# Optimization experiments

Measured on AMD Instinct MI355X. Metric: run time of the kernel, lower is better.

The kernel has to match this reference:

```python
import jax, jax.numpy as jnp
import numpy as np

N = 50000      # nodes
E = 800000     # edges
D_IN = 128
D_H = 128
D_OUT = 64


def _glorot(key, fan_in, fan_out):
    s = float(np.sqrt(6.0 / (fan_in + fan_out)))
    return jax.random.uniform(key, (fan_in, fan_out), jnp.float32, -s, s)


def setup_inputs() -> dict:
    key = jax.random.key(0)
    ks = jax.random.split(key, 8)
    x = jax.random.normal(ks[0], (N, D_IN), jnp.float32)
    edge_index = jax.random.randint(ks[1], (2, E), 0, N, dtype=jnp.int32)
    return {
        "x": x,
        "edge_index": edge_index,
        "W0": _glorot(ks[2], D_IN, D_H), "b0": jnp.zeros((D_H,), jnp.float32),
        "W1": _glorot(ks[3], D_H, D_H),  "b1": jnp.zeros((D_H,), jnp.float32),
        "W2": _glorot(ks[4], D_H, D_H),  "b2": jnp.zeros((D_H,), jnp.float32),
        "W_out": _glorot(ks[5], D_H, D_OUT), "b_out": jnp.zeros((D_OUT,), jnp.float32),
    }


def reference(x, edge_index, W0, b0, W1, b1, W2, b2, W_out, b_out):
    src = edge_index[0]
    dst = edge_index[1]
    # GCN normalization with self-loops: deg = in-degree(dst) + 1
    deg = jax.ops.segment_sum(jnp.ones((E,), x.dtype), dst, num_segments=N) + 1.0
    dinv = jax.lax.rsqrt(deg)                       # [N]
    edge_coef = (dinv[src] * dinv[dst])[:, None]    # [E,1]
    self_coef = (dinv * dinv)[:, None]              # [N,1]

    def gcn_conv(h, W, b):
        h = h @ W                                            # [N,F]
        agg = jax.ops.segment_sum(h[src] * edge_coef, dst, num_segments=N)
        agg = agg + h * self_coef                            # self-loop term
        return agg + b

    h = x
    for W, b in ((W0, b0), (W1, b1), (W2, b2)):
        h_in = h
        h = jax.nn.relu(gcn_conv(h, W, b))  # eval mode: dropout is identity
        if h.shape == h_in.shape:
            h = h + h_in
    return h @ W_out + b_out
```

## Files before the change

### kernel.cpp

```cpp
#include <hip/hip_runtime.h>

#define N_NODES 50000
#define N_EDGES 800000
#define NBUCKET 98

static inline int cdiv(int a, int b) { return (a + b - 1) / b; }

typedef __attribute__((ext_vector_type(8))) short s8vec;
typedef __attribute__((ext_vector_type(4))) float f32x4;

__device__ inline ushort f2b(float f) {
    uint u = __float_as_uint(f);
    uint r = (u + 0x7fffu + ((u >> 16) & 1u)) >> 16;
    return (ushort)r;
}
__device__ inline float b2f_lo(uint v) { return __uint_as_float(v << 16); }
__device__ inline float b2f_hi(uint v) { return __uint_as_float(v & 0xffff0000u); }

__device__ inline void add8(float* acc, uint4 v) {
    acc[0] += b2f_lo(v.x); acc[1] += b2f_hi(v.x);
    acc[2] += b2f_lo(v.y); acc[3] += b2f_hi(v.y);
    acc[4] += b2f_lo(v.z); acc[5] += b2f_hi(v.z);
    acc[6] += b2f_lo(v.w); acc[7] += b2f_hi(v.w);
}


__global__ __launch_bounds__(256) void k_prep(int* cnt,
                                              const float* __restrict__ W0, const float* __restrict__ W1,
                                              const float* __restrict__ W2, const float* __restrict__ Wo,
                                              ushort* Wt0, ushort* Wt1, ushort* Wt2, ushort* Wto) {
    int b = blockIdx.x;
    if (b < 196) {
        int i = b * 256 + threadIdx.x;
        if (i < N_NODES) cnt[i] = 0;
        return;
    }
    int i = (b - 196) * 256 + threadIdx.x;
    if (i < 16384) {
        int nn = i >> 7, k = i & 127;
        Wt0[i] = f2b(W0[k * 128 + nn]);
    } else if (i < 32768) {
        int j = i - 16384; int nn = j >> 7, k = j & 127;
        Wt1[j] = f2b(W1[k * 128 + nn]);
    } else if (i < 49152) {
        int j = i - 32768; int nn = j >> 7, k = j & 127;
        Wt2[j] = f2b(W2[k * 128 + nn]);
    } else if (i < 57344) {
        int j = i - 49152; int nn = j >> 7, k = j & 127;
        Wto[j] = f2b(Wo[k * 64 + nn]);
    }
}

__global__ __launch_bounds__(256) void k_count(const int* __restrict__ dst, int* cnt, int e) {
    int i = blockIdx.x * 256 + threadIdx.x;
    if (i < e) atomicAdd(&cnt[dst[i]], 1);
}


__global__ __launch_bounds__(512) void k_scan_all(const int* __restrict__ cnt,
                                                  int* rowptr, int* cursor, float* dinv,
                                                  int* bcur, int n, int e, int nb) {
    __shared__ int sh[512];
    int t = threadIdx.x, b = blockIdx.x;
    int start = b * 512;

    int partial = 0;
    for (int i = t; i < start; i += 512) partial += cnt[i];
    sh[t] = partial;
    __syncthreads();
    for (int off = 256; off > 0; off >>= 1) {
        if (t < off) sh[t] += sh[t + off];
        __syncthreads();
    }
    int base = sh[0];
    __syncthreads();

    int i = start + t;
    int v = (i < n) ? cnt[i] : 0;
    sh[t] = v;
    __syncthreads();
    for (int off = 1; off < 512; off <<= 1) {
        int add = (t >= off) ? sh[t - off] : 0;
        __syncthreads();
        sh[t] += add;
        __syncthreads();
    }
    if (i < n) {
        int rp = base + sh[t] - v;
        rowptr[i] = rp;
        cursor[i] = rp;
        dinv[i] = rsqrtf((float)v + 1.0f);
    }
    if (t == 0) bcur[b] = base;
    if (b == nb - 1 && t == 0) rowptr[n] = e;
}


template <int NCOL, bool IN_F32, bool OUT_F32, bool SCALE>
__device__ inline void mm_body(const void* __restrict__ Av, const ushort* __restrict__ Wt,
                               const float* __restrict__ bias, const float* __restrict__ dinv,
                               void* __restrict__ Cv, int n, int bid) {
    constexpr int NT = NCOL / 16;
    int wave = threadIdx.x >> 6;
    int lane = threadIdx.x & 63;
    int quad = lane >> 4;
    int lm = lane & 15;
    int row0 = bid * 128 + wave * 32;

    int rA0 = row0 + lm;      if (rA0 > n - 1) rA0 = n - 1;
    int rA1 = row0 + 16 + lm; if (rA1 > n - 1) rA1 = n - 1;

    f32x4 acc[2][NT];
#pragma unroll
    for (int r = 0; r < 2; r++)
#pragma unroll
        for (int t = 0; t < NT; t++) acc[r][t] = (f32x4){0.f, 0.f, 0.f, 0.f};

    for (int kc = 0; kc < 128; kc += 32) {
        s8vec af[2];
        if (IN_F32) {
            const float* A = (const float*)Av;
#pragma unroll
            for (int r = 0; r < 2; r++) {
                const float* p = A + (size_t)(r ? rA1 : rA0) * 128 + quad * 8 + kc;
                float4 a = *(const float4*)p, b = *(const float4*)(p + 4);
                s8vec v;
                v[0] = (short)f2b(a.x); v[1] = (short)f2b(a.y);
                v[2] = (short)f2b(a.z); v[3] = (short)f2b(a.w);
                v[4] = (short)f2b(b.x); v[5] = (short)f2b(b.y);
                v[6] = (short)f2b(b.z); v[7] = (short)f2b(b.w);
                af[r] = v;
            }
        } else {
            const ushort* A = (const ushort*)Av;
            af[0] = *(const s8vec*)(A + (size_t)rA0 * 128 + quad * 8 + kc);
            af[1] = *(const s8vec*)(A + (size_t)rA1 * 128 + quad * 8 + kc);
        }
#pragma unroll
        for (int t = 0; t < NT; t++) {
            s8vec bf = *(const s8vec*)(Wt + (size_t)(t * 16 + lm) * 128 + kc + quad * 8);
            acc[0][t] = __builtin_amdgcn_mfma_f32_16x16x32_bf16(af[0], bf, acc[0][t], 0, 0, 0);
            acc[1][t] = __builtin_amdgcn_mfma_f32_16x16x32_bf16(af[1], bf, acc[1][t], 0, 0, 0);
        }
    }

#pragma unroll
    for (int r = 0; r < 2; r++) {
#pragma unroll
        for (int i = 0; i < 4; i++) {
            int rr = row0 + r * 16 + quad * 4 + i;
            if (rr < n) {
                float dv = SCALE ? dinv[rr] : 1.0f;
#pragma unroll
                for (int t = 0; t < NT; t++) {
                    int col = t * 16 + lm;
                    if (OUT_F32)
                        ((float*)Cv)[(size_t)rr * NCOL + col] = acc[r][t][i] + bias[col];
                    else
                        ((ushort*)Cv)[(size_t)rr * 128 + col] =
                            f2b(SCALE ? acc[r][t][i] * dv : acc[r][t][i]);
                }
            }
        }
    }
}

template <int NCOL, bool IN_F32, bool OUT_F32, bool SCALE>
__global__ __launch_bounds__(256) void k_mm(const void* __restrict__ Av,
                                            const ushort* __restrict__ Wt,
                                            const float* __restrict__ bias,
                                            const float* __restrict__ dinv,
                                            void* __restrict__ Cv, int n) {
    mm_body<NCOL, IN_F32, OUT_F32, SCALE>(Av, Wt, bias, dinv, Cv, n, blockIdx.x);
}

__global__ __launch_bounds__(256) void k_mm0_fillA(const void* __restrict__ Av,
                                                   const ushort* __restrict__ Wt,
                                                   const float* __restrict__ dinv,
                                                   void* __restrict__ Cv, int n, int mmblocks,
                                                   const int* __restrict__ src, const int* __restrict__ dst,
                                                   int* bcur, uint2* pairs, int e) {
    __shared__ int hist[NBUCKET], gb[NBUCKET];
    if ((int)blockIdx.x >= mmblocks) {
        int e0 = ((int)blockIdx.x - mmblocks) * 2048;
        if (threadIdx.x < NBUCKET) hist[threadIdx.x] = 0;
        __syncthreads();
        int sarr[8], darr[8], offr[8];
#pragma unroll
        for (int k = 0; k < 8; k++) {
            int i = e0 + k * 256 + threadIdx.x;
            int s = 0, d = 0, o = -1;
            if (i < e) {
                s = src[i]; d = dst[i];
                o = atomicAdd(&hist[d >> 9], 1);
            }
            sarr[k] = s; darr[k] = d; offr[k] = o;
        }
        __syncthreads();
        if (threadIdx.x < NBUCKET)
            gb[threadIdx.x] = atomicAdd(&bcur[threadIdx.x], hist[threadIdx.x]);
        __syncthreads();
#pragma unroll
        for (int k = 0; k < 8; k++) {
            if (offr[k] >= 0) {
                int pos = gb[darr[k] >> 9] + offr[k];
                pairs[pos] = make_uint2((uint)sarr[k], (uint)darr[k]);
            }
        }
        return;
    }
    mm_body<128, true, false, true>(Av, Wt, nullptr, dinv, Cv, n, blockIdx.x);
}

__global__ __launch_bounds__(256) void k_fillB(const uint2* __restrict__ pairs,
                                               int* cursor, uint* ed, int e) {
    int i0 = blockIdx.x * 2048 + threadIdx.x;
#pragma unroll
    for (int k = 0; k < 8; k++) {
        int i = i0 + k * 256;
        if (i < e) {
            uint2 p = pairs[i];
            int pos = atomicAdd(&cursor[p.y], 1);
            ed[pos] = p.x;
        }
    }
}


template <bool RES_F32>
__global__ __launch_bounds__(256) void k_gatherb(const uint4* __restrict__ T4,
                                                 const int* __restrict__ rowptr,
                                                 const uint* __restrict__ ed,
                                                 const float* __restrict__ dinv,
                                                 const float* __restrict__ bias,
                                                 const void* __restrict__ resv,
                                                 uint4* __restrict__ out4, int n) {
    int node = blockIdx.x * 16 + (threadIdx.x >> 4);
    if (node >= n) return;
    int ql = threadIdx.x & 15;
    int qb = threadIdx.x & 48;

    float acc[8] = {0.f, 0.f, 0.f, 0.f, 0.f, 0.f, 0.f, 0.f};
    int beg = rowptr[node], end = rowptr[node + 1];

    for (int base = beg; base < end; base += 16) {
        int m = end - base; if (m > 16) m = 16;
        int idx = base + ql; if (idx > end - 1) idx = end - 1;
        uint em = ed[idx];
        int j = 0;
        for (; j + 8 <= m; j += 8) {
            int s0 = __shfl((int)em, qb + j);
            int s1 = __shfl((int)em, qb + j + 1);
            int s2 = __shfl((int)em, qb + j + 2);
            int s3 = __shfl((int)em, qb + j + 3);
            int s4 = __shfl((int)em, qb + j + 4);
            int s5 = __shfl((int)em, qb + j + 5);
            int s6 = __shfl((int)em, qb + j + 6);
            int s7 = __shfl((int)em, qb + j + 7);
            uint4 v0 = T4[(size_t)s0 * 16 + ql];
            uint4 v1 = T4[(size_t)s1 * 16 + ql];
            uint4 v2 = T4[(size_t)s2 * 16 + ql];
            uint4 v3 = T4[(size_t)s3 * 16 + ql];
            uint4 v4 = T4[(size_t)s4 * 16 + ql];
            uint4 v5 = T4[(size_t)s5 * 16 + ql];
            uint4 v6 = T4[(size_t)s6 * 16 + ql];
            uint4 v7 = T4[(size_t)s7 * 16 + ql];
            add8(acc, v0); add8(acc, v1); add8(acc, v2); add8(acc, v3);
            add8(acc, v4); add8(acc, v5); add8(acc, v6); add8(acc, v7);
        }
        for (; j + 4 <= m; j += 4) {
            int s0 = __shfl((int)em, qb + j);
            int s1 = __shfl((int)em, qb + j + 1);
            int s2 = __shfl((int)em, qb + j + 2);
            int s3 = __shfl((int)em, qb + j + 3);
            uint4 v0 = T4[(size_t)s0 * 16 + ql];
            uint4 v1 = T4[(size_t)s1 * 16 + ql];
            uint4 v2 = T4[(size_t)s2 * 16 + ql];
            uint4 v3 = T4[(size_t)s3 * 16 + ql];
            add8(acc, v0); add8(acc, v1); add8(acc, v2); add8(acc, v3);
        }
        for (; j < m; j++) {
            int s = __shfl((int)em, qb + j);
            uint4 v = T4[(size_t)s * 16 + ql];
            add8(acc, v);
        }
    }

    uint4 vs = T4[(size_t)node * 16 + ql];
    add8(acc, vs);

    float di = dinv[node];
    float4 bv0 = ((const float4*)bias)[ql * 2];
    float4 bv1 = ((const float4*)bias)[ql * 2 + 1];
    float bb[8] = {bv0.x, bv0.y, bv0.z, bv0.w, bv1.x, bv1.y, bv1.z, bv1.w};

    float r[8];
    if (RES_F32) {
        float4 r0 = ((const float4*)resv)[(size_t)node * 32 + ql * 2];
        float4 r1 = ((const float4*)resv)[(size_t)node * 32 + ql * 2 + 1];
        r[0] = r0.x; r[1] = r0.y; r[2] = r0.z; r[3] = r0.w;
        r[4] = r1.x; r[5] = r1.y; r[6] = r1.z; r[7] = r1.w;
    } else {
        uint4 rv = ((const uint4*)resv)[(size_t)node * 16 + ql];
        r[0] = b2f_lo(rv.x); r[1] = b2f_hi(rv.x); r[2] = b2f_lo(rv.y); r[3] = b2f_hi(rv.y);
        r[4] = b2f_lo(rv.z); r[5] = b2f_hi(rv.z); r[6] = b2f_lo(rv.w); r[7] = b2f_hi(rv.w);
    }

    float o[8];
#pragma unroll
    for (int i = 0; i < 8; i++)
        o[i] = fmaxf(acc[i] * di + bb[i], 0.f) + r[i];

    uint4 ov;
    ov.x = (uint)f2b(o[0]) | ((uint)f2b(o[1]) << 16);
    ov.y = (uint)f2b(o[2]) | ((uint)f2b(o[3]) << 16);
    ov.z = (uint)f2b(o[4]) | ((uint)f2b(o[5]) << 16);
    ov.w = (uint)f2b(o[6]) | ((uint)f2b(o[7]) << 16);
    out4[(size_t)node * 16 + ql] = ov;
}


extern "C" void kernel_launch(void* const* d_in, const int* in_sizes, int n_in,
                              void* d_out, int out_size, void* d_ws, size_t ws_size,
                              hipStream_t stream) {
    const float* x  = (const float*)d_in[0];
    const int* eidx = (const int*)d_in[1];
    const float* W0 = (const float*)d_in[2];
    const float* b0 = (const float*)d_in[3];
    const float* W1 = (const float*)d_in[4];
    const float* b1 = (const float*)d_in[5];
    const float* W2 = (const float*)d_in[6];
    const float* b2 = (const float*)d_in[7];
    const float* Wo = (const float*)d_in[8];
    const float* bo = (const float*)d_in[9];
    float* out = (float*)d_out;

    const int N = N_NODES, E = N_EDGES;
    const int* srcI = eidx;
    const int* dstI = eidx + E;

    char* ws = (char*)d_ws;
    auto alloc = [&](size_t bytes) { char* p = ws; ws += (bytes + 255) / 256 * 256; return p; };
    int*    cnt    = (int*)alloc((size_t)N * 4);
    int*    cursor = (int*)alloc((size_t)N * 4);
    int*    rowptr = (int*)alloc((size_t)(N + 1) * 4);
    int*    bcur   = (int*)alloc((size_t)NBUCKET * 4);
    float*  dinv   = (float*)alloc((size_t)N * 4);
    uint*   ed     = (uint*)alloc((size_t)E * 4);
    uint2*  pairs  = (uint2*)alloc((size_t)E * 8);
    ushort* tmpb   = (ushort*)alloc((size_t)N * 128 * 2);
    ushort* hAb    = (ushort*)alloc((size_t)N * 128 * 2);
    ushort* hBb    = (ushort*)alloc((size_t)N * 128 * 2);
    ushort* Wt0    = (ushort*)alloc(128 * 128 * 2);
    ushort* Wt1    = (ushort*)alloc(128 * 128 * 2);
    ushort* Wt2    = (ushort*)alloc(128 * 128 * 2);
    ushort* Wto    = (ushort*)alloc(64 * 128 * 2);

    dim3 b256(256), b512(512);

    const int mmGrid   = cdiv(N, 128);
    const int fillGrid = cdiv(E, 2048);
    const int gGrid    = cdiv(N, 16);

    k_prep<<<196 + 224, b256, 0, stream>>>(cnt, W0, W1, W2, Wo, Wt0, Wt1, Wt2, Wto);
    k_count<<<cdiv(E, 256), b256, 0, stream>>>(dstI, cnt, E);
    k_scan_all<<<NBUCKET, b512, 0, stream>>>(cnt, rowptr, cursor, dinv, bcur, N, E, NBUCKET);

    k_mm0_fillA<<<mmGrid + fillGrid, b256, 0, stream>>>(x, Wt0, dinv, tmpb, N, mmGrid,
                                                        srcI, dstI, bcur, pairs, E);
    k_fillB<<<fillGrid, b256, 0, stream>>>(pairs, cursor, ed, E);
    k_gatherb<true><<<gGrid, b256, 0, stream>>>((const uint4*)tmpb, rowptr, ed, dinv, b0, x, (uint4*)hAb, N);

    k_mm<128, false, false, true><<<mmGrid, b256, 0, stream>>>(hAb, Wt1, nullptr, dinv, tmpb, N);
    k_gatherb<false><<<gGrid, b256, 0, stream>>>((const uint4*)tmpb, rowptr, ed, dinv, b1, hAb, (uint4*)hBb, N);

    k_mm<128, false, false, true><<<mmGrid, b256, 0, stream>>>(hBb, Wt2, nullptr, dinv, tmpb, N);
    k_gatherb<false><<<gGrid, b256, 0, stream>>>((const uint4*)tmpb, rowptr, ed, dinv, b2, hBb, (uint4*)hAb, N);

    k_mm<64, false, true, false><<<mmGrid, b256, 0, stream>>>(hAb, Wto, bo, dinv, out, N);
}
```

Baseline: 322.9 us.

## Replace bucketed two-pass CSR fill with direct atomic scatter; shrink GEMM tiles

Edge CSR construction now scatters source ids directly via atomics on per-node cursors inside the fused mm0 launch. This removes the bucket histogram pass, the intermediate pairs buffer and the separate fill kernel. The dense GEMM tile is also halved to one 16-row MFMA tile per wave, doubling the grid. This trades lost reuse of weight fragments and more scattered, less coherent writes for fewer kernels and less memory traffic.

```diff
diff --git a/kernel.cpp b/kernel.cpp
--- a/kernel.cpp
+++ b/kernel.cpp
@@ -2,7 +2,7 @@
 
 #define N_NODES 50000
 #define N_EDGES 800000
-#define NBUCKET 98
+#define NB512 98
 
 static inline int cdiv(int a, int b) { return (a + b - 1) / b; }
 
@@ -59,7 +59,7 @@
 
 __global__ __launch_bounds__(512) void k_scan_all(const int* __restrict__ cnt,
                                                   int* rowptr, int* cursor, float* dinv,
-                                                  int* bcur, int n, int e, int nb) {
+                                                  int n, int e, int nb) {
     __shared__ int sh[512];
     int t = threadIdx.x, b = blockIdx.x;
     int start = b * 512;
@@ -91,7 +91,6 @@
         cursor[i] = rp;
         dinv[i] = rsqrtf((float)v + 1.0f);
     }
-    if (t == 0) bcur[b] = base;
     if (b == nb - 1 && t == 0) rowptr[n] = e;
 }
 
@@ -105,61 +104,48 @@
     int lane = threadIdx.x & 63;
     int quad = lane >> 4;
     int lm = lane & 15;
-    int row0 = bid * 128 + wave * 32;
-
-    int rA0 = row0 + lm;      if (rA0 > n - 1) rA0 = n - 1;
-    int rA1 = row0 + 16 + lm; if (rA1 > n - 1) rA1 = n - 1;
-
-    f32x4 acc[2][NT];
-#pragma unroll
-    for (int r = 0; r < 2; r++)
-#pragma unroll
-        for (int t = 0; t < NT; t++) acc[r][t] = (f32x4){0.f, 0.f, 0.f, 0.f};
+    int row0 = bid * 64 + wave * 16;
+
+    int rA = row0 + lm; if (rA > n - 1) rA = n - 1;
+
+    f32x4 acc[NT];
+#pragma unroll
+    for (int t = 0; t < NT; t++) acc[t] = (f32x4){0.f, 0.f, 0.f, 0.f};
 
     for (int kc = 0; kc < 128; kc += 32) {
-        s8vec af[2];
+        s8vec af;
         if (IN_F32) {
-            const float* A = (const float*)Av;
-#pragma unroll
-            for (int r = 0; r < 2; r++) {
-                const float* p = A + (size_t)(r ? rA1 : rA0) * 128 + quad * 8 + kc;
-                float4 a = *(const float4*)p, b = *(const float4*)(p + 4);
-                s8vec v;
-                v[0] = (short)f2b(a.x); v[1] = (short)f2b(a.y);
-                v[2] = (short)f2b(a.z); v[3] = (short)f2b(a.w);
-                v[4] = (short)f2b(b.x); v[5] = (short)f2b(b.y);
-                v[6] = (short)f2b(b.z); v[7] = (short)f2b(b.w);
-                af[r] = v;
-            }
+            const float* p = (const float*)Av + (size_t)rA * 128 + quad * 8 + kc;
+            float4 a = *(const float4*)p, b = *(const float4*)(p + 4);
+            s8vec v;
+            v[0] = (short)f2b(a.x); v[1] = (short)f2b(a.y);
+            v[2] = (short)f2b(a.z); v[3] = (short)f2b(a.w);
+            v[4] = (short)f2b(b.x); v[5] = (short)f2b(b.y);
+            v[6] = (short)f2b(b.z); v[7] = (short)f2b(b.w);
+            af = v;
         } else {
-            const ushort* A = (const ushort*)Av;
-            af[0] = *(const s8vec*)(A + (size_t)rA0 * 128 + quad * 8 + kc);
-            af[1] = *(const s8vec*)(A + (size_t)rA1 * 128 + quad * 8 + kc);
+            af = *(const s8vec*)((const ushort*)Av + (size_t)rA * 128 + quad * 8 + kc);
         }
 #pragma unroll
         for (int t = 0; t < NT; t++) {
             s8vec bf = *(const s8vec*)(Wt + (size_t)(t * 16 + lm) * 128 + kc + quad * 8);
-            acc[0][t] = __builtin_amdgcn_mfma_f32_16x16x32_bf16(af[0], bf, acc[0][t], 0, 0, 0);
-            acc[1][t] = __builtin_amdgcn_mfma_f32_16x16x32_bf16(af[1], bf, acc[1][t], 0, 0, 0);
-        }
-    }
-
-#pragma unroll
-    for (int r = 0; r < 2; r++) {
-#pragma unroll
-        for (int i = 0; i < 4; i++) {
-            int rr = row0 + r * 16 + quad * 4 + i;
-            if (rr < n) {
-                float dv = SCALE ? dinv[rr] : 1.0f;
-#pragma unroll
-                for (int t = 0; t < NT; t++) {
-                    int col = t * 16 + lm;
-                    if (OUT_F32)
-                        ((float*)Cv)[(size_t)rr * NCOL + col] = acc[r][t][i] + bias[col];
-                    else
-                        ((ushort*)Cv)[(size_t)rr * 128 + col] =
-                            f2b(SCALE ? acc[r][t][i] * dv : acc[r][t][i]);
-                }
+            acc[t] = __builtin_amdgcn_mfma_f32_16x16x32_bf16(af, bf, acc[t], 0, 0, 0);
+        }
+    }
+
+#pragma unroll
+    for (int i = 0; i < 4; i++) {
+        int rr = row0 + quad * 4 + i;
+        if (rr < n) {
+            float dv = SCALE ? dinv[rr] : 1.0f;
+#pragma unroll
+            for (int t = 0; t < NT; t++) {
+                int col = t * 16 + lm;
+                if (OUT_F32)
+                    ((float*)Cv)[(size_t)rr * NCOL + col] = acc[t][i] + bias[col];
+                else
+                    ((ushort*)Cv)[(size_t)rr * 128 + col] =
+                        f2b(SCALE ? acc[t][i] * dv : acc[t][i]);
             }
         }
     }
@@ -174,56 +160,26 @@
     mm_body<NCOL, IN_F32, OUT_F32, SCALE>(Av, Wt, bias, dinv, Cv, n, blockIdx.x);
 }
 
-__global__ __launch_bounds__(256) void k_mm0_fillA(const void* __restrict__ Av,
-                                                   const ushort* __restrict__ Wt,
-                                                   const float* __restrict__ dinv,
-                                                   void* __restrict__ Cv, int n, int mmblocks,
-                                                   const int* __restrict__ src, const int* __restrict__ dst,
-                                                   int* bcur, uint2* pairs, int e) {
-    __shared__ int hist[NBUCKET], gb[NBUCKET];
+__global__ __launch_bounds__(256) void k_mm0_fill(const void* __restrict__ Av,
+                                                  const ushort* __restrict__ Wt,
+                                                  const float* __restrict__ dinv,
+                                                  void* __restrict__ Cv, int n, int mmblocks,
+                                                  const int* __restrict__ src, const int* __restrict__ dst,
+                                                  int* cursor, uint* ed, int e) {
     if ((int)blockIdx.x >= mmblocks) {
-        int e0 = ((int)blockIdx.x - mmblocks) * 2048;
-        if (threadIdx.x < NBUCKET) hist[threadIdx.x] = 0;
-        __syncthreads();
-        int sarr[8], darr[8], offr[8];
-#pragma unroll
-        for (int k = 0; k < 8; k++) {
-            int i = e0 + k * 256 + threadIdx.x;
-            int s = 0, d = 0, o = -1;
+        int base = ((int)blockIdx.x - mmblocks) * 1024 + threadIdx.x;
+#pragma unroll
+        for (int k = 0; k < 4; k++) {
+            int i = base + k * 256;
             if (i < e) {
-                s = src[i]; d = dst[i];
-                o = atomicAdd(&hist[d >> 9], 1);
+                int d = dst[i], s = src[i];
+                int pos = atomicAdd(&cursor[d], 1);
+                __builtin_nontemporal_store((uint)s, &ed[pos]);
             }
-            sarr[k] = s; darr[k] = d; offr[k] = o;
-        }
-        __syncthreads();
-        if (threadIdx.x < NBUCKET)
-            gb[threadIdx.x] = atomicAdd(&bcur[threadIdx.x], hist[threadIdx.x]);
-        __syncthreads();
-#pragma unroll
-        for (int k = 0; k < 8; k++) {
-            if (offr[k] >= 0) {
-                int pos = gb[darr[k] >> 9] + offr[k];
-                pairs[pos] = make_uint2((uint)sarr[k], (uint)darr[k]);
-            }
         }
         return;
     }
     mm_body<128, true, false, true>(Av, Wt, nullptr, dinv, Cv, n, blockIdx.x);
-}
-
-__global__ __launch_bounds__(256) void k_fillB(const uint2* __restrict__ pairs,
-                                               int* cursor, uint* ed, int e) {
-    int i0 = blockIdx.x * 2048 + threadIdx.x;
-#pragma unroll
-    for (int k = 0; k < 8; k++) {
-        int i = i0 + k * 256;
-        if (i < e) {
-            uint2 p = pairs[i];
-            int pos = atomicAdd(&cursor[p.y], 1);
-            ed[pos] = p.x;
-        }
-    }
 }
 
 
@@ -344,10 +300,8 @@
     int*    cnt    = (int*)alloc((size_t)N * 4);
     int*    cursor = (int*)alloc((size_t)N * 4);
     int*    rowptr = (int*)alloc((size_t)(N + 1) * 4);
-    int*    bcur   = (int*)alloc((size_t)NBUCKET * 4);
     float*  dinv   = (float*)alloc((size_t)N * 4);
     uint*   ed     = (uint*)alloc((size_t)E * 4);
-    uint2*  pairs  = (uint2*)alloc((size_t)E * 8);
     ushort* tmpb   = (ushort*)alloc((size_t)N * 128 * 2);
     ushort* hAb    = (ushort*)alloc((size_t)N * 128 * 2);
     ushort* hBb    = (ushort*)alloc((size_t)N * 128 * 2);
@@ -358,17 +312,16 @@
 
     dim3 b256(256), b512(512);
 
-    const int mmGrid   = cdiv(N, 128);
-    const int fillGrid = cdiv(E, 2048);
+    const int mmGrid   = cdiv(N, 64);
+    const int fillGrid = cdiv(E, 1024);
     const int gGrid    = cdiv(N, 16);
 
     k_prep<<<196 + 224, b256, 0, stream>>>(cnt, W0, W1, W2, Wo, Wt0, Wt1, Wt2, Wto);
     k_count<<<cdiv(E, 256), b256, 0, stream>>>(dstI, cnt, E);
-    k_scan_all<<<NBUCKET, b512, 0, stream>>>(cnt, rowptr, cursor, dinv, bcur, N, E, NBUCKET);
-
-    k_mm0_fillA<<<mmGrid + fillGrid, b256, 0, stream>>>(x, Wt0, dinv, tmpb, N, mmGrid,
-                                                        srcI, dstI, bcur, pairs, E);
-    k_fillB<<<fillGrid, b256, 0, stream>>>(pairs, cursor, ed, E);
+    k_scan_all<<<NB512, b512, 0, stream>>>(cnt, rowptr, cursor, dinv, N, E, NB512);
+
+    k_mm0_fill<<<mmGrid + fillGrid, b256, 0, stream>>>(x, Wt0, dinv, tmpb, N, mmGrid,
+                                                       srcI, dstI, cursor, ed, E);
     k_gatherb<true><<<gGrid, b256, 0, stream>>>((const uint4*)tmpb, rowptr, ed, dinv, b0, x, (uint4*)hAb, N);
 
     k_mm<128, false, false, true><<<mmGrid, b256, 0, stream>>>(hAb, Wt1, nullptr, dinv, tmpb, N);
```

After: 365.6 us. +13.2%, slower.
